# Performance work log

Hardware: AMD Instinct MI355X
Metric: run time of the kernel (lower is better)

## Reference

```python
import jax, jax.numpy as jnp
import numpy as np

B, N, D, E, A, DIAM = 16, 1024, 128, 16384, 64, 3


def setup_inputs() -> dict:
    key = jax.random.key(0)
    ks = jax.random.split(key, 20)
    s = 0.05
    inp = {
        "node_features": jax.random.normal(ks[0], (B, N, D), jnp.float32),
        "edge_features": jax.random.normal(ks[1], (B, N, N), jnp.float32),
        "src_idx": jax.random.randint(ks[2], (E,), 0, N, jnp.int32),
        "tgt_idx": jax.random.randint(ks[3], (E,), 0, N, jnp.int32),
        # message MLP: Linear(2D+1 -> D)
        "W_msg": jax.random.normal(ks[4], (2 * D + 1, D), jnp.float32) * s,
        "b_msg": jax.random.normal(ks[5], (D,), jnp.float32) * s,
        # GRUCell(D, D), gate order r,z,n (torch convention)
        "W_ih": jax.random.normal(ks[6], (3 * D, D), jnp.float32) * s,
        "W_hh": jax.random.normal(ks[7], (3 * D, D), jnp.float32) * s,
        "b_ih": jax.random.normal(ks[8], (3 * D,), jnp.float32) * s,
        "b_hh": jax.random.normal(ks[9], (3 * D,), jnp.float32) * s,
        # readout: Linear(D,D)+SELU, Linear(D,D)+SELU, then policy head Linear(D,A)
        "W_r1": jax.random.normal(ks[10], (D, D), jnp.float32) * s,
        "b_r1": jax.random.normal(ks[11], (D,), jnp.float32) * s,
        "W_r2": jax.random.normal(ks[12], (D, D), jnp.float32) * s,
        "b_r2": jax.random.normal(ks[13], (D,), jnp.float32) * s,
        "W_pol": jax.random.normal(ks[14], (D, A), jnp.float32) * s,
        "b_pol": jax.random.normal(ks[15], (A,), jnp.float32) * s,
    }
    return inp


def reference(node_features, edge_features, src_idx, tgt_idx,
              W_msg, b_msg, W_ih, W_hh, b_ih, b_hh,
              W_r1, b_r1, W_r2, b_r2, W_pol, b_pol):
    h = node_features  # [B, N, D]
    ef = edge_features[:, src_idx, tgt_idx][..., None]  # [B, E, 1], constant across rounds
    for _ in range(DIAM):
        src_f = h[:, src_idx]  # [B, E, D] gather
        tgt_f = h[:, tgt_idx]  # [B, E, D]
        comb = jnp.concatenate([src_f, tgt_f, ef], axis=-1)  # [B, E, 2D+1]
        msg = jax.nn.selu(comb @ W_msg + b_msg)  # [B, E, D]
        # scatter-sum messages onto target nodes
        agg = jax.vmap(lambda m: jax.ops.segment_sum(m, tgt_idx, num_segments=N))(msg)  # [B, N, D]
        # GRUCell update (torch math, gate order r,z,n; b_hn stays inside r*(...))
        gi = agg @ W_ih.T + b_ih  # [B, N, 3D]
        gh = h @ W_hh.T + b_hh    # [B, N, 3D]
        i_r, i_z, i_n = jnp.split(gi, 3, axis=-1)
        h_r, h_z, h_n = jnp.split(gh, 3, axis=-1)
        r = jax.nn.sigmoid(i_r + h_r)
        z = jax.nn.sigmoid(i_z + h_z)
        n = jnp.tanh(i_n + r * h_n)
        h = (1.0 - z) * n + z * h
    pooled = h.sum(axis=1)  # [B, D]
    pooled = jax.nn.selu(pooled @ W_r1 + b_r1)
    pooled = jax.nn.selu(pooled @ W_r2 + b_r2)
    return pooled @ W_pol + b_pol  # [B, A] policy logits
```

## Files before the change

kernel.cpp:

```cpp
#include <hip/hip_runtime.h>
#include <hip/hip_bf16.h>
#include <math.h>

constexpr int kB = 16;
constexpr int kN = 1024;
constexpr int kD = 128;
constexpr int kE = 16384;

typedef short bf16x8 __attribute__((ext_vector_type(8)));
typedef float f32x4 __attribute__((ext_vector_type(4)));
typedef unsigned short us4 __attribute__((ext_vector_type(4)));

__device__ __forceinline__ float selu_f(float x) {
    const float scale = 1.0507009873554805f;
    const float alpha = 1.6732632423543772f;
    return x > 0.f ? scale * x : scale * alpha * (__expf(x) - 1.f);
}

__device__ __forceinline__ float sigmoid_f(float x) {
    return __builtin_amdgcn_rcpf(1.f + __expf(-x));
}

__device__ __forceinline__ float tanh_f(float x) {
    return 1.f - 2.f * __builtin_amdgcn_rcpf(1.f + __expf(2.f * x));
}

__device__ __forceinline__ float bf2f(unsigned short u) {
    union { unsigned int i; float f; } x;
    x.i = ((unsigned int)u) << 16;
    return x.f;
}

__device__ __forceinline__ unsigned short f2bf(float f) {
    union { float f; unsigned int i; } u;
    u.f = f;
    const unsigned int r = u.i + 0x7fffu + ((u.i >> 16) & 1u);
    return (unsigned short)(r >> 16);
}

__global__ void k_h0cw(const float* __restrict__ nodef, unsigned short* __restrict__ h_bf,
                       const int* __restrict__ tgt, int* __restrict__ cnt,
                       int* __restrict__ rank,
                       const float* __restrict__ Wmsg, const float* __restrict__ Whh,
                       const float* __restrict__ Wih,
                       const float* __restrict__ bih, const float* __restrict__ bhh,
                       unsigned short* __restrict__ WcatT,
                       unsigned short* __restrict__ Wfused,
                       float* __restrict__ bihP, float* __restrict__ bhhP) {
    const int bid = blockIdx.x;
    const int t = threadIdx.x;
    if (bid < 2048) {
        const int gid = bid * 256 + t;
        const float4 v = ((const float4*)nodef)[gid];
        us4 o;
        o.x = f2bf(v.x);
        o.y = f2bf(v.y);
        o.z = f2bf(v.z);
        o.w = f2bf(v.w);
        ((us4*)h_bf)[gid] = o;
        if (gid < kE) rank[gid] = atomicAdd(&cnt[tgt[gid]], 1);
    } else {
        const int j = (bid - 2048) * 2 + (t >> 7);
        const int k = t & 127;
        if (j < 256) {
            float v = (j < 128) ? Wmsg[k * 128 + j] : Wmsg[(128 + k) * 128 + (j - 128)];
            WcatT[j * 128 + k] = f2bf(v);
        } else {
            const int f = j - 256;
            const int dg = f / 48, rem = f % 48;
            const int g = rem / 16, di = rem % 16;
            const int orig = g * 128 + dg * 16 + di;
            Wfused[(size_t)f * 256 + k] = f2bf(Wih[(size_t)orig * 128 + k]);
            Wfused[(size_t)f * 256 + 128 + k] = f2bf(Whh[(size_t)orig * 128 + k]);
            if (k == 0) {
                bihP[f] = bih[orig];
                bhhP[f] = bhh[orig];
            }
        }
    }
}

__launch_bounds__(1024)
__global__ void k_scan(const int* __restrict__ cnt, int* __restrict__ rowstart) {
    __shared__ int wsum[16];
    const int t = threadIdx.x;
    const int lane = t & 63, wv = t >> 6;
    const int v = cnt[t];
    int x = v;
#pragma unroll
    for (int off = 1; off < 64; off <<= 1) {
        const int y = __shfl_up(x, off, 64);
        if (lane >= off) x += y;
    }
    if (lane == 63) wsum[wv] = x;
    __syncthreads();
    if (wv == 0 && lane < 16) {
        const int s = wsum[lane];
        int xs = s;
#pragma unroll
        for (int off = 1; off < 16; off <<= 1) {
            const int y = __shfl_up(xs, off, 64);
            if (lane >= off) xs += y;
        }
        wsum[lane] = xs - s;
    }
    __syncthreads();
    const int incl = x + wsum[wv];
    rowstart[t] = incl - v;
    if (t == kN - 1) rowstart[kN] = incl;
}

__global__ void k_sct(const int* __restrict__ src, const int* __restrict__ tgt,
                      const int* __restrict__ rank, const int* __restrict__ rowstart,
                      int* __restrict__ ssrc, int* __restrict__ stgt) {
    const int e = blockIdx.x * 256 + threadIdx.x;
    const int tg = tgt[e];
    const int pos = rowstart[tg] + rank[e];
    ssrc[pos] = src[e];
    stgt[pos] = tg;
}

__global__ void k_gather_ef(const float* __restrict__ edgef, const int* __restrict__ ssrc,
                            const int* __restrict__ stgt, float* __restrict__ efg) {
    const int gid = blockIdx.x * 256 + threadIdx.x;
    const int b = gid >> 14;
    const int i = gid & (kE - 1);
    efg[gid] = edgef[(size_t)b * kN * kN + (size_t)ssrc[i] * kN + stgt[i]];
}

__launch_bounds__(256)
__global__ void k_mm256(const unsigned short* __restrict__ A,
                        const unsigned short* __restrict__ Bt,
                        unsigned short* __restrict__ HST) {
    __shared__ uint4 As[2048];
    __shared__ uint4 Bs[2048];
    const int t = threadIdx.x;
    const int r0 = blockIdx.x * 128;
    const int c0 = blockIdx.y * 128;
    const uint4* gA = (const uint4*)(A + (size_t)r0 * 128);
    const uint4* gB = (const uint4*)(Bt + (size_t)c0 * 128);
#pragma unroll
    for (int i = 0; i < 8; ++i) {
        const int f = i * 256 + t;
        const int row = f >> 4, c16 = f & 15;
        const int d = row * 16 + (c16 ^ (row & 7));
        As[d] = gA[f];
        Bs[d] = gB[f];
    }
    __syncthreads();
    const int w = t >> 6, l = t & 63;
    const int wm = (w & 1) * 64, wn = (w >> 1) * 64;
    const int lin = l & 15, kq = l >> 4;
    f32x4 acc[4][4] = {};
#pragma unroll
    for (int s = 0; s < 4; ++s) {
        bf16x8 a[4], b[4];
#pragma unroll
        for (int mi = 0; mi < 4; ++mi) {
            const int row = wm + mi * 16 + lin;
            a[mi] = *(const bf16x8*)&As[row * 16 + ((s * 4 + kq) ^ (row & 7))];
        }
#pragma unroll
        for (int ni = 0; ni < 4; ++ni) {
            const int row = wn + ni * 16 + lin;
            b[ni] = *(const bf16x8*)&Bs[row * 16 + ((s * 4 + kq) ^ (row & 7))];
        }
#pragma unroll
        for (int mi = 0; mi < 4; ++mi)
#pragma unroll
            for (int ni = 0; ni < 4; ++ni)
                acc[mi][ni] = __builtin_amdgcn_mfma_f32_16x16x32_bf16(
                    b[ni], a[mi], acc[mi][ni], 0, 0, 0);
    }
    const int rq = kq * 4;
#pragma unroll
    for (int mi = 0; mi < 4; ++mi) {
        const int row = r0 + wm + mi * 16 + lin;
#pragma unroll
        for (int ni = 0; ni < 4; ++ni) {
            const int col = c0 + wn + ni * 16 + rq;
            us4 o;
            o.x = f2bf(acc[mi][ni][0]);
            o.y = f2bf(acc[mi][ni][1]);
            o.z = f2bf(acc[mi][ni][2]);
            o.w = f2bf(acc[mi][ni][3]);
            *(us4*)&HST[(size_t)row * 256 + col] = o;
        }
    }
}

__launch_bounds__(256)
__global__ void k_edge(const unsigned short* __restrict__ HST, const float* __restrict__ efg,
                       const int* __restrict__ ssrc, const int* __restrict__ rowstart,
                       const float* __restrict__ Wmsg, const float* __restrict__ bmsg,
                       unsigned short* __restrict__ agg_bf) {
    __shared__ float4 part[2][4][32];
    const int t = threadIdx.x;
    const int b = blockIdx.y;
    const int tl = t >> 7;
    const int tg = blockIdx.x * 2 + tl;
    const int slot = (t >> 5) & 3;
    const int lane = t & 31;
    const int c = lane * 4;
    const float4 w3 = *(const float4*)&Wmsg[256 * 128 + c];
    const float4 bm = *(const float4*)&bmsg[c];
    const size_t base = (size_t)b * kN;
    const us4 htu = *(const us4*)&HST[(base + tg) * 256 + 128 + c];
    const float hb0 = bf2f(htu.x) + bm.x;
    const float hb1 = bf2f(htu.y) + bm.y;
    const float hb2 = bf2f(htu.z) + bm.z;
    const float hb3 = bf2f(htu.w) + bm.w;
    const float* efb = efg + b * kE;
    const int j0 = rowstart[tg], j1 = rowstart[tg + 1];
    float a0 = 0.f, a1 = 0.f, a2 = 0.f, a3 = 0.f;
    for (int j = j0 + slot; j < j1; j += 4) {
        const int s = ssrc[j];
        const float ef = efb[j];
        const us4 hs = *(const us4*)&HST[(base + s) * 256 + c];
        a0 += selu_f(bf2f(hs.x) + fmaf(ef, w3.x, hb0));
        a1 += selu_f(bf2f(hs.y) + fmaf(ef, w3.y, hb1));
        a2 += selu_f(bf2f(hs.z) + fmaf(ef, w3.z, hb2));
        a3 += selu_f(bf2f(hs.w) + fmaf(ef, w3.w, hb3));
    }
    part[tl][slot][lane] = make_float4(a0, a1, a2, a3);
    __syncthreads();
    if (slot == 0) {
        const float4 p1 = part[tl][1][lane];
        const float4 p2 = part[tl][2][lane];
        const float4 p3 = part[tl][3][lane];
        a0 += p1.x + p2.x + p3.x;
        a1 += p1.y + p2.y + p3.y;
        a2 += p1.z + p2.z + p3.z;
        a3 += p1.w + p2.w + p3.w;
        us4 o;
        o.x = f2bf(a0);
        o.y = f2bf(a1);
        o.z = f2bf(a2);
        o.w = f2bf(a3);
        *(us4*)&agg_bf[(base + tg) * 128 + c] = o;
    }
}

__launch_bounds__(256)
__global__ void k_gigru(const unsigned short* __restrict__ agg_bf,
                        const unsigned short* __restrict__ h_bf_in,
                        const unsigned short* __restrict__ Wfused,
                        const float* __restrict__ bihP, const float* __restrict__ bhhP,
                        unsigned short* __restrict__ h_bf_out,
                        float* __restrict__ pooled, int lastIter) {
    __shared__ uint4 As[2048];
    __shared__ uint4 Bs[1536];
    const int t = threadIdx.x;
    const int r0 = blockIdx.x * 128;
    const int y = blockIdx.y;
    const int w = t >> 6, l = t & 63;
    const int wm = (w & 1) * 64, wc0 = (w >> 1) * 48;
    const int lin = l & 15, kq = l >> 4, rq = kq * 4;
    f32x4 acc[4][3] = {};
    f32x4 accN[4] = {};
#pragma unroll
    for (int stage = 0; stage < 2; ++stage) {
        const unsigned short* Ap = stage ? h_bf_in : agg_bf;
        const uint4* gA = (const uint4*)(Ap + (size_t)r0 * 128);
#pragma unroll
        for (int i = 0; i < 8; ++i) {
            const int f = i * 256 + t;
            const int row = f >> 4, c16 = f & 15;
            As[row * 16 + (c16 ^ (row & 7))] = gA[f];
        }
        const uint4* gW = (const uint4*)Wfused;
#pragma unroll
        for (int i = 0; i < 6; ++i) {
            const int f = i * 256 + t;
            const int j = f >> 4, c16 = f & 15;
            Bs[j * 16 + (c16 ^ (j & 7))] = gW[(size_t)(y * 96 + j) * 32 + stage * 16 + c16];
        }
        __syncthreads();
#pragma unroll
        for (int ks = 0; ks < 4; ++ks) {
            bf16x8 a[4], b[3];
#pragma unroll
            for (int mi = 0; mi < 4; ++mi) {
                const int row = wm + mi * 16 + lin;
                a[mi] = *(const bf16x8*)&As[row * 16 + ((ks * 4 + kq) ^ (row & 7))];
            }
#pragma unroll
            for (int ni = 0; ni < 3; ++ni) {
                const int row = wc0 + ni * 16 + lin;
                b[ni] = *(const bf16x8*)&Bs[row * 16 + ((ks * 4 + kq) ^ (row & 7))];
            }
#pragma unroll
            for (int mi = 0; mi < 4; ++mi) {
                acc[mi][0] = __builtin_amdgcn_mfma_f32_16x16x32_bf16(a[mi], b[0], acc[mi][0], 0, 0, 0);
                acc[mi][1] = __builtin_amdgcn_mfma_f32_16x16x32_bf16(a[mi], b[1], acc[mi][1], 0, 0, 0);
                if (stage == 0)
                    acc[mi][2] = __builtin_amdgcn_mfma_f32_16x16x32_bf16(a[mi], b[2], acc[mi][2], 0, 0, 0);
                else
                    accN[mi] = __builtin_amdgcn_mfma_f32_16x16x32_bf16(a[mi], b[2], accN[mi], 0, 0, 0);
            }
        }
        __syncthreads();
    }
    const int colR = y * 96 + wc0 + lin;
    const float bR = bihP[colR] + bhhP[colR];
    const float bZ = bihP[colR + 16] + bhhP[colR + 16];
    const float biN = bihP[colR + 32];
    const float bhN = bhhP[colR + 32];
    const int dgg = y * 2 + (wc0 / 48);
    const int d = dgg * 16 + lin;
    const int bb = r0 >> 10;
    const int dc = d >> 3, de = d & 7;
    float psum = 0.f;
#pragma unroll
    for (int mi = 0; mi < 4; ++mi) {
#pragma unroll
        for (int r = 0; r < 4; ++r) {
            const int rowL = wm + mi * 16 + rq + r;
            const float rr = sigmoid_f(acc[mi][0][r] + bR);
            const float zz = sigmoid_f(acc[mi][1][r] + bZ);
            const float i_n = acc[mi][2][r] + biN;
            const float h_n = accN[mi][r] + bhN;
            const float nn = tanh_f(fmaf(rr, h_n, i_n));
            const float hv = bf2f(((const unsigned short*)&As[rowL * 16 + (dc ^ (rowL & 7))])[de]);
            const float o = fmaf(zz, hv - nn, nn);
            h_bf_out[(size_t)(r0 + rowL) * 128 + d] = f2bf(o);
            psum += o;
        }
    }
    if (lastIter) atomicAdd(&pooled[bb * 128 + d], psum);
}

__global__ void k_head(const float* __restrict__ pooled,
                       const float* __restrict__ Wr1, const float* __restrict__ br1,
                       const float* __restrict__ Wr2, const float* __restrict__ br2,
                       const float* __restrict__ Wpol, const float* __restrict__ bpol,
                       float* __restrict__ out) {
    __shared__ float p[128], t1[128];
    const int b = blockIdx.x, d = threadIdx.x;
    p[d] = pooled[b * 128 + d];
    __syncthreads();
    float acc = br1[d];
    for (int k = 0; k < 128; ++k) acc = fmaf(p[k], Wr1[k * 128 + d], acc);
    t1[d] = selu_f(acc);
    __syncthreads();
    acc = br2[d];
    for (int k = 0; k < 128; ++k) acc = fmaf(t1[k], Wr2[k * 128 + d], acc);
    __syncthreads();
    p[d] = selu_f(acc);
    __syncthreads();
    if (d < 64) {
        float o = bpol[d];
        for (int k = 0; k < 128; ++k) o = fmaf(p[k], Wpol[k * 64 + d], o);
        out[b * 64 + d] = o;
    }
}

extern "C" void kernel_launch(void* const* d_in, const int* in_sizes, int n_in,
                              void* d_out, int out_size, void* d_ws, size_t ws_size,
                              hipStream_t stream) {
    const float* nodef = (const float*)d_in[0];
    const float* edgef = (const float*)d_in[1];
    const int* src = (const int*)d_in[2];
    const int* tgt = (const int*)d_in[3];
    const float* Wmsg = (const float*)d_in[4];
    const float* bmsg = (const float*)d_in[5];
    const float* Wih = (const float*)d_in[6];
    const float* Whh = (const float*)d_in[7];
    const float* bih = (const float*)d_in[8];
    const float* bhh = (const float*)d_in[9];
    const float* Wr1 = (const float*)d_in[10];
    const float* br1 = (const float*)d_in[11];
    const float* Wr2 = (const float*)d_in[12];
    const float* br2 = (const float*)d_in[13];
    const float* Wpol = (const float*)d_in[14];
    const float* bpol = (const float*)d_in[15];
    float* out = (float*)d_out;

    float* ws = (float*)d_ws;
    float* efg = ws;
    float* bihP = efg + 262144;
    float* bhhP = bihP + 384;
    int* cnt = (int*)(bhhP + 384);
    float* pooled = (float*)(cnt + 1024);
    unsigned short* HST = (unsigned short*)(pooled + 2048);
    unsigned short* hbfA = HST + 4194304;
    unsigned short* hbfB = hbfA + 2097152;
    unsigned short* agg_bf = hbfB + 2097152;
    unsigned short* WcatT = agg_bf + 2097152;
    unsigned short* Wfused = WcatT + 32768;
    int* stgt = (int*)(Wfused + 98304);
    int* rowstart = stgt + 16384;
    int* ssrc = rowstart + 1040;
    int* rank = ssrc + 16384;

    hipMemsetAsync(cnt, 0, (1024 + 2048) * sizeof(int), stream);
    k_h0cw<<<2048 + 320, 256, 0, stream>>>(nodef, hbfA, tgt, cnt, rank, Wmsg, Whh, Wih,
                                           bih, bhh, WcatT, Wfused, bihP, bhhP);
    k_scan<<<1, 1024, 0, stream>>>(cnt, rowstart);
    k_sct<<<kE / 256, 256, 0, stream>>>(src, tgt, rank, rowstart, ssrc, stgt);
    k_gather_ef<<<(kB * kE) / 256, 256, 0, stream>>>(edgef, ssrc, stgt, efg);

    for (int it = 0; it < 3; ++it) {
        unsigned short* hcur = (it & 1) ? hbfB : hbfA;
        unsigned short* hnxt = (it & 1) ? hbfA : hbfB;
        k_mm256<<<dim3(128, 2), 256, 0, stream>>>(hcur, WcatT, HST);
        k_edge<<<dim3(kN / 2, kB), 256, 0, stream>>>(HST, efg, ssrc, rowstart, Wmsg, bmsg, agg_bf);
        k_gigru<<<dim3(128, 4), 256, 0, stream>>>(agg_bf, hcur, Wfused, bihP, bhhP, hnxt,
                                                  pooled, it == 2 ? 1 : 0);
    }

    k_head<<<kB, 128, 0, stream>>>(pooled, Wr1, br1, Wr2, br2, Wpol, bpol, out);
}
```

Baseline: 272.6 us.

## Fuse edge scatter with ef gather, widen edge lanes, reduce pooled atomics in LDS

Merges the edge-sort scatter and the edge-feature gather into one kernel, so a launch and the stgt array round trip go away. The edge kernel now has each lane handle 8 channels with 16-byte loads and uses 8 edge slots per target instead of 4, which means more loads in flight per node. The last GRU iteration first reduces the pooled sums through LDS atomics, then issues far fewer global atomics. The cost is more registers in the edge kernel and an extra LDS reduction step.

```diff
diff --git a/kernel.cpp b/kernel.cpp
--- a/kernel.cpp
+++ b/kernel.cpp
@@ -9,7 +9,9 @@
 
 typedef short bf16x8 __attribute__((ext_vector_type(8)));
 typedef float f32x4 __attribute__((ext_vector_type(4)));
+typedef float f32x8 __attribute__((ext_vector_type(8)));
 typedef unsigned short us4 __attribute__((ext_vector_type(4)));
+typedef unsigned short us8 __attribute__((ext_vector_type(8)));
 
 __device__ __forceinline__ float selu_f(float x) {
     const float scale = 1.0507009873554805f;
@@ -110,22 +112,18 @@
     if (t == kN - 1) rowstart[kN] = incl;
 }
 
-__global__ void k_sct(const int* __restrict__ src, const int* __restrict__ tgt,
-                      const int* __restrict__ rank, const int* __restrict__ rowstart,
-                      int* __restrict__ ssrc, int* __restrict__ stgt) {
-    const int e = blockIdx.x * 256 + threadIdx.x;
+__global__ void k_sctg(const float* __restrict__ edgef, const int* __restrict__ src,
+                       const int* __restrict__ tgt, const int* __restrict__ rank,
+                       const int* __restrict__ rowstart,
+                       int* __restrict__ ssrc, float* __restrict__ efg) {
+    const int gid = blockIdx.x * 256 + threadIdx.x;
+    const int b = gid >> 14;
+    const int e = gid & (kE - 1);
     const int tg = tgt[e];
     const int pos = rowstart[tg] + rank[e];
-    ssrc[pos] = src[e];
-    stgt[pos] = tg;
-}
-
-__global__ void k_gather_ef(const float* __restrict__ edgef, const int* __restrict__ ssrc,
-                            const int* __restrict__ stgt, float* __restrict__ efg) {
-    const int gid = blockIdx.x * 256 + threadIdx.x;
-    const int b = gid >> 14;
-    const int i = gid & (kE - 1);
-    efg[gid] = edgef[(size_t)b * kN * kN + (size_t)ssrc[i] * kN + stgt[i]];
+    const int s = src[e];
+    efg[b * kE + pos] = edgef[(size_t)b * kN * kN + (size_t)s * kN + tg];
+    if (b == 0) ssrc[pos] = s;
 }
 
 __launch_bounds__(256)
@@ -194,50 +192,45 @@
                        const int* __restrict__ ssrc, const int* __restrict__ rowstart,
                        const float* __restrict__ Wmsg, const float* __restrict__ bmsg,
                        unsigned short* __restrict__ agg_bf) {
-    __shared__ float4 part[2][4][32];
+    __shared__ float part[2][8][16][8];
     const int t = threadIdx.x;
     const int b = blockIdx.y;
     const int tl = t >> 7;
     const int tg = blockIdx.x * 2 + tl;
-    const int slot = (t >> 5) & 3;
-    const int lane = t & 31;
-    const int c = lane * 4;
-    const float4 w3 = *(const float4*)&Wmsg[256 * 128 + c];
-    const float4 bm = *(const float4*)&bmsg[c];
+    const int r = t & 127;
+    const int lane = r & 15;
+    const int slot = r >> 4;
+    const int c = lane * 8;
+    const f32x8 w3 = *(const f32x8*)&Wmsg[256 * 128 + c];
+    const f32x8 bm = *(const f32x8*)&bmsg[c];
     const size_t base = (size_t)b * kN;
-    const us4 htu = *(const us4*)&HST[(base + tg) * 256 + 128 + c];
-    const float hb0 = bf2f(htu.x) + bm.x;
-    const float hb1 = bf2f(htu.y) + bm.y;
-    const float hb2 = bf2f(htu.z) + bm.z;
-    const float hb3 = bf2f(htu.w) + bm.w;
+    const us8 htu = *(const us8*)&HST[(base + tg) * 256 + 128 + c];
+    float hb[8];
+#pragma unroll
+    for (int k = 0; k < 8; ++k) hb[k] = bf2f(htu[k]) + bm[k];
     const float* efb = efg + b * kE;
     const int j0 = rowstart[tg], j1 = rowstart[tg + 1];
-    float a0 = 0.f, a1 = 0.f, a2 = 0.f, a3 = 0.f;
-    for (int j = j0 + slot; j < j1; j += 4) {
+    float a[8] = {};
+    for (int j = j0 + slot; j < j1; j += 8) {
         const int s = ssrc[j];
         const float ef = efb[j];
-        const us4 hs = *(const us4*)&HST[(base + s) * 256 + c];
-        a0 += selu_f(bf2f(hs.x) + fmaf(ef, w3.x, hb0));
-        a1 += selu_f(bf2f(hs.y) + fmaf(ef, w3.y, hb1));
-        a2 += selu_f(bf2f(hs.z) + fmaf(ef, w3.z, hb2));
-        a3 += selu_f(bf2f(hs.w) + fmaf(ef, w3.w, hb3));
-    }
-    part[tl][slot][lane] = make_float4(a0, a1, a2, a3);
+        const us8 hs = *(const us8*)&HST[(base + s) * 256 + c];
+#pragma unroll
+        for (int k = 0; k < 8; ++k)
+            a[k] += selu_f(bf2f(hs[k]) + fmaf(ef, w3[k], hb[k]));
+    }
+#pragma unroll
+    for (int k = 0; k < 8; ++k) part[tl][slot][lane][k] = a[k];
     __syncthreads();
     if (slot == 0) {
-        const float4 p1 = part[tl][1][lane];
-        const float4 p2 = part[tl][2][lane];
-        const float4 p3 = part[tl][3][lane];
-        a0 += p1.x + p2.x + p3.x;
-        a1 += p1.y + p2.y + p3.y;
-        a2 += p1.z + p2.z + p3.z;
-        a3 += p1.w + p2.w + p3.w;
-        us4 o;
-        o.x = f2bf(a0);
-        o.y = f2bf(a1);
-        o.z = f2bf(a2);
-        o.w = f2bf(a3);
-        *(us4*)&agg_bf[(base + tg) * 128 + c] = o;
+#pragma unroll
+        for (int s2 = 1; s2 < 8; ++s2)
+#pragma unroll
+            for (int k = 0; k < 8; ++k) a[k] += part[tl][s2][lane][k];
+        us8 o;
+#pragma unroll
+        for (int k = 0; k < 8; ++k) o[k] = f2bf(a[k]);
+        *(us8*)&agg_bf[(base + tg) * 128 + c] = o;
     }
 }
 
@@ -250,6 +243,7 @@
                         float* __restrict__ pooled, int lastIter) {
     __shared__ uint4 As[2048];
     __shared__ uint4 Bs[1536];
+    __shared__ float psums[32];
     const int t = threadIdx.x;
     const int r0 = blockIdx.x * 128;
     const int y = blockIdx.y;
@@ -327,7 +321,17 @@
             psum += o;
         }
     }
-    if (lastIter) atomicAdd(&pooled[bb * 128 + d], psum);
+    if (lastIter) {
+        const int ld = (wc0 / 48) * 16 + lin;
+        if (t < 32) psums[t] = 0.f;
+        __syncthreads();
+        atomicAdd(&psums[ld], psum);
+        __syncthreads();
+        if (t < 32) {
+            const int d2 = (y * 2 + (t >> 4)) * 16 + (t & 15);
+            atomicAdd(&pooled[bb * 128 + d2], psums[t]);
+        }
+    }
 }
 
 __global__ void k_head(const float* __restrict__ pooled,
@@ -388,8 +392,7 @@
     unsigned short* agg_bf = hbfB + 2097152;
     unsigned short* WcatT = agg_bf + 2097152;
     unsigned short* Wfused = WcatT + 32768;
-    int* stgt = (int*)(Wfused + 98304);
-    int* rowstart = stgt + 16384;
+    int* rowstart = (int*)(Wfused + 98304);
     int* ssrc = rowstart + 1040;
     int* rank = ssrc + 16384;
 
@@ -397,8 +400,7 @@
     k_h0cw<<<2048 + 320, 256, 0, stream>>>(nodef, hbfA, tgt, cnt, rank, Wmsg, Whh, Wih,
                                            bih, bhh, WcatT, Wfused, bihP, bhhP);
     k_scan<<<1, 1024, 0, stream>>>(cnt, rowstart);
-    k_sct<<<kE / 256, 256, 0, stream>>>(src, tgt, rank, rowstart, ssrc, stgt);
-    k_gather_ef<<<(kB * kE) / 256, 256, 0, stream>>>(edgef, ssrc, stgt, efg);
+    k_sctg<<<(kB * kE) / 256, 256, 0, stream>>>(edgef, src, tgt, rank, rowstart, ssrc, efg);
 
     for (int it = 0; it < 3; ++it) {
         unsigned short* hcur = (it & 1) ? hbfB : hbfA;
```

New measurement: 259.2 us. 4.9% less time.
